# Optimization experiments

Hardware: AMD Instinct MI355X
Metric: run time of the kernel (lower is better)

Reference implementation:

```python
import jax, jax.numpy as jnp
import numpy as np

GAMMA = 0.5

def smooth_step(t, gamma=GAMMA):
    # DSelect-k SmoothStep: 0 below -g/2, 1 above g/2, cubic in between.
    tc = jnp.clip(t, -gamma / 2, gamma / 2)
    return (-2.0 / gamma**3) * tc**3 + (3.0 / (2.0 * gamma)) * tc + 0.5

def setup_inputs() -> dict:
    key = jax.random.key(0)
    k1, k2, k3 = jax.random.split(key, 3)
    B, p, k, m = 65536, 1024, 8, 6
    x = jax.random.normal(k1, (B, p), dtype=jnp.float32)
    G_w = jax.random.normal(k2, (k, p), dtype=jnp.float32) / np.sqrt(p)
    G_b = jnp.zeros((k,), dtype=jnp.float32)
    W_w = jax.random.normal(k3, (k * m, p), dtype=jnp.float32) / np.sqrt(p)
    W_b = jnp.zeros((k * m,), dtype=jnp.float32)
    return {"x": x, "G_w": G_w, "G_b": G_b, "W_w": W_w, "W_b": W_b}

def reference(x, G_w, G_b, W_w, W_b):
    B = x.shape[0]
    k = G_w.shape[0]
    m = W_w.shape[0] // k
    n = 2 ** m  # number of experts encoded by m binary gates
    gates = (x @ W_w.T + W_b).reshape(B, k, m)
    z = smooth_step(gates)  # (B, k, m) in [0, 1]
    # per_example_selector: probability of expert e = prod_j (z_j if bit_j(e) else 1-z_j)
    bits = ((np.arange(n)[:, None] >> np.arange(m)[None, :]) & 1).astype(bool)  # (n, m)
    bits = jnp.asarray(bits)
    sel = jnp.prod(jnp.where(bits[None, None, :, :], z[:, :, None, :], 1.0 - z[:, :, None, :]), axis=-1)  # (B, k, n)
    weights = jax.nn.softmax(x @ G_w.T + G_b, axis=1)  # (B, k)
    mixture = jnp.einsum('bk,bkn->bn', weights, sel)  # bmm((B,1,k),(B,k,n)) -> (B, n)
    return mixture
```

## Files before the change

kernel.cpp:

```cpp
#include <hip/hip_runtime.h>

typedef _Float16 half8 __attribute__((ext_vector_type(8)));
typedef float f32x4 __attribute__((ext_vector_type(4)));
typedef float f4 __attribute__((ext_vector_type(4)));

#define P_DIM 1024
#define BM 64
#define NH 8
#define AF_ROW 132

__global__ __launch_bounds__(256) void prep_weights(
    const float* __restrict__ Gw, const float* __restrict__ Gb,
    const float* __restrict__ Ww, const float* __restrict__ Wb,
    _Float16* __restrict__ Wf2, float* __restrict__ biasC) {
  int i = blockIdx.x * 256 + threadIdx.x;
  int j = i & 7;
  int l = (i >> 3) & 63;
  int t = (i >> 9) & 3;
  int S = i >> 11;
  int row = t * 16 + (l & 15);
  int k   = S * 32 + (l >> 4) * 8 + j;
  float v = 0.0f;
  if (row < 48) v = Ww[row * P_DIM + k];
  else if (row < 56) v = Gw[(row - 48) * P_DIM + k];
  Wf2[i] = (_Float16)v;
  if (i < 64) {
    float bv = 0.0f;
    if (i < 48) bv = Wb[i];
    else if (i < 56) bv = Gb[i - 48];
    biasC[i] = bv;
  }
}

#define BODY(cc) do { \
    half8 b0_ = *(const half8*)(BsR + (size_t)((2*(cc)  )*4    ) * 1024); \
    half8 b1_ = *(const half8*)(BsR + (size_t)((2*(cc)+1)*4    ) * 1024); \
    half8 b2_ = *(const half8*)(BsR + (size_t)((2*(cc)  )*4 + 1) * 1024); \
    half8 b3_ = *(const half8*)(BsR + (size_t)((2*(cc)+1)*4 + 1) * 1024); \
    f4 a0_[4], a1_[4]; \
    { const char* p0 = Abase0 + (cc) * 256; \
      a0_[0] = *(const f4*)(p0);       a0_[1] = *(const f4*)(p0 + 16); \
      a0_[2] = *(const f4*)(p0 + 128); a0_[3] = *(const f4*)(p0 + 144); \
      const char* p1 = Abase1 + (cc) * 256; \
      a1_[0] = *(const f4*)(p1);       a1_[1] = *(const f4*)(p1 + 16); \
      a1_[2] = *(const f4*)(p1 + 128); a1_[3] = *(const f4*)(p1 + 144); } \
    half8 h00_, h01_, h10_, h11_; \
    h00_[0]=(_Float16)a0_[0][0]; h00_[1]=(_Float16)a0_[0][1]; h00_[2]=(_Float16)a0_[0][2]; h00_[3]=(_Float16)a0_[0][3]; \
    h00_[4]=(_Float16)a0_[1][0]; h00_[5]=(_Float16)a0_[1][1]; h00_[6]=(_Float16)a0_[1][2]; h00_[7]=(_Float16)a0_[1][3]; \
    h01_[0]=(_Float16)a0_[2][0]; h01_[1]=(_Float16)a0_[2][1]; h01_[2]=(_Float16)a0_[2][2]; h01_[3]=(_Float16)a0_[2][3]; \
    h01_[4]=(_Float16)a0_[3][0]; h01_[5]=(_Float16)a0_[3][1]; h01_[6]=(_Float16)a0_[3][2]; h01_[7]=(_Float16)a0_[3][3]; \
    h10_[0]=(_Float16)a1_[0][0]; h10_[1]=(_Float16)a1_[0][1]; h10_[2]=(_Float16)a1_[0][2]; h10_[3]=(_Float16)a1_[0][3]; \
    h10_[4]=(_Float16)a1_[1][0]; h10_[5]=(_Float16)a1_[1][1]; h10_[6]=(_Float16)a1_[1][2]; h10_[7]=(_Float16)a1_[1][3]; \
    h11_[0]=(_Float16)a1_[2][0]; h11_[1]=(_Float16)a1_[2][1]; h11_[2]=(_Float16)a1_[2][2]; h11_[3]=(_Float16)a1_[2][3]; \
    h11_[4]=(_Float16)a1_[3][0]; h11_[5]=(_Float16)a1_[3][1]; h11_[6]=(_Float16)a1_[3][2]; h11_[7]=(_Float16)a1_[3][3]; \
    acc[0] = __builtin_amdgcn_mfma_f32_16x16x32_f16(h00_, b0_, acc[0], 0, 0, 0); \
    acc[0] = __builtin_amdgcn_mfma_f32_16x16x32_f16(h01_, b1_, acc[0], 0, 0, 0); \
    acc[1] = __builtin_amdgcn_mfma_f32_16x16x32_f16(h00_, b2_, acc[1], 0, 0, 0); \
    acc[1] = __builtin_amdgcn_mfma_f32_16x16x32_f16(h01_, b3_, acc[1], 0, 0, 0); \
    acc[2] = __builtin_amdgcn_mfma_f32_16x16x32_f16(h10_, b0_, acc[2], 0, 0, 0); \
    acc[2] = __builtin_amdgcn_mfma_f32_16x16x32_f16(h11_, b1_, acc[2], 0, 0, 0); \
    acc[3] = __builtin_amdgcn_mfma_f32_16x16x32_f16(h10_, b2_, acc[3], 0, 0, 0); \
    acc[3] = __builtin_amdgcn_mfma_f32_16x16x32_f16(h11_, b3_, acc[3], 0, 0, 0); \
  } while (0)

__global__ __launch_bounds__(256, 3) void fused_gate(
    const float* __restrict__ x, const _Float16* __restrict__ Wf2,
    const float* __restrict__ biasC, float* __restrict__ out) {
  __shared__ __align__(16) float Af[BM][AF_ROW];
  __shared__ __align__(16) _Float16 BsH[8192];

  const int tid  = threadIdx.x;
  const int lane = tid & 63;
  const int w    = tid >> 6;
  const int row0 = blockIdx.x * BM;
  const int l15  = lane & 15;
  const int q    = lane >> 4;

  const int mrow = (w >> 1) * 32;
  const int ncol = (w & 1) * 32;
  const int tb   = (w & 1) * 2;

  const char* xg = (const char*)(x + (size_t)(row0 + w * 16) * P_DIM) + lane * 8;
  const char* bgG = (const char*)Wf2 + (size_t)(w * 4) * 1024 + lane * 16;

  char* Aw = (char*)&Af[w * 16][0] + lane * 8;
  const char* Abase0 = (const char*)&Af[mrow + l15][0] + q * 32;
  const char* Abase1 = Abase0 + 16 * 528;
  char* BsW = (char*)BsH + (size_t)(w * 4) * 1024 + lane * 16;
  const char* BsR = (const char*)BsH + (size_t)tb * 1024 + lane * 16;

  f32x4 acc[4];
#pragma unroll
  for (int t = 0; t < 4; ++t) acc[t] = (f32x4){0.f, 0.f, 0.f, 0.f};

  float2 pf[16];
#pragma unroll
  for (int i = 0; i < 16; ++i) pf[i] = *(const float2*)(xg + i * 4096);
  half8 bR[4];
#pragma unroll
  for (int i = 0; i < 4; ++i) bR[i] = *(const half8*)(bgG + (size_t)i * 1024);

  for (int h = 0; h < NH; ++h) {
    if (h) __syncthreads();
#pragma unroll
    for (int i = 0; i < 16; ++i)
      *(float2*)(Aw + i * 528) = pf[i];
#pragma unroll
    for (int i = 0; i < 4; ++i)
      *(half8*)(BsW + (size_t)i * 1024) = bR[i];
    __syncthreads();
    if (h + 1 < NH) {
      const size_t boff = (size_t)(h + 1) * 16384;
#pragma unroll
      for (int i = 0; i < 4; ++i)
        bR[i] = *(const half8*)(bgG + boff + (size_t)i * 1024);
#pragma unroll
      for (int i = 0; i < 16; ++i)
        pf[i] = *(const float2*)(xg + i * 4096 + (h + 1) * 512);
    }
    BODY(0);
    BODY(1);
  }

  __syncthreads();
  float (*S)[65] = (float (*)[65])&Af[0][0];

#pragma unroll
  for (int m = 0; m < 2; ++m) {
#pragma unroll
    for (int j = 0; j < 2; ++j) {
      const int col = ncol + j * 16 + l15;
      float bias = biasC[col];
#pragma unroll
      for (int rr = 0; rr < 4; ++rr) {
        S[mrow + m * 16 + q * 4 + rr][col] = acc[m * 2 + j][rr] + bias;
      }
    }
  }
  __syncthreads();

  const int r2  = tid >> 2;
  const int sub = tid & 3;

  float lg[8];
#pragma unroll
  for (int k = 0; k < 8; ++k) lg[k] = S[r2][48 + k];
  float mx = lg[0];
#pragma unroll
  for (int k = 1; k < 8; ++k) mx = fmaxf(mx, lg[k]);
  float wk[8];
  float ssum = 0.f;
#pragma unroll
  for (int k = 0; k < 8; ++k) { wk[k] = expf(lg[k] - mx); ssum += wk[k]; }
  const float inv = 1.0f / ssum;

  float mix[16];
#pragma unroll
  for (int i = 0; i < 16; ++i) mix[i] = 0.f;

#pragma unroll
  for (int k = 0; k < 8; ++k) {
    float z[6];
#pragma unroll
    for (int j = 0; j < 6; ++j) {
      float tt = S[r2][k * 6 + j];
      float tc = fminf(fmaxf(tt, -0.25f), 0.25f);
      z[j] = fmaf(tc, fmaf(-16.0f * tc, tc, 3.0f), 0.5f);
    }
    float f4v = (sub & 1) ? z[4] : 1.0f - z[4];
    float f5v = (sub & 2) ? z[5] : 1.0f - z[5];
    float wf = wk[k] * inv * f4v * f5v;
    float t2[2], t4[4], t8[8], t16[16];
    t2[0] = 1.0f - z[0]; t2[1] = z[0];
#pragma unroll
    for (int i = 0; i < 2; ++i) { t4[i] = t2[i] * (1.0f - z[1]); t4[i + 2] = t2[i] * z[1]; }
#pragma unroll
    for (int i = 0; i < 4; ++i) { t8[i] = t4[i] * (1.0f - z[2]); t8[i + 4] = t4[i] * z[2]; }
#pragma unroll
    for (int i = 0; i < 8; ++i) { t16[i] = t8[i] * (1.0f - z[3]); t16[i + 8] = t8[i] * z[3]; }
#pragma unroll
    for (int i = 0; i < 16; ++i) mix[i] = fmaf(wf, t16[i], mix[i]);
  }

  float* op = out + (size_t)(row0 + r2) * 64 + sub * 16;
#pragma unroll
  for (int g = 0; g < 4; ++g) {
    float4 o;
    o.x = mix[4 * g + 0]; o.y = mix[4 * g + 1];
    o.z = mix[4 * g + 2]; o.w = mix[4 * g + 3];
    ((float4*)op)[g] = o;
  }
}

extern "C" void kernel_launch(void* const* d_in, const int* in_sizes, int n_in,
                              void* d_out, int out_size, void* d_ws, size_t ws_size,
                              hipStream_t stream) {
  const float* x  = (const float*)d_in[0];
  const float* Gw = (const float*)d_in[1];
  const float* Gb = (const float*)d_in[2];
  const float* Ww = (const float*)d_in[3];
  const float* Wb = (const float*)d_in[4];
  float* out = (float*)d_out;

  _Float16* Wf2  = (_Float16*)d_ws;
  float*    bias = (float*)((char*)d_ws + 64 * P_DIM * sizeof(_Float16));

  const int B = in_sizes[0] / P_DIM;

  prep_weights<<<dim3(256), dim3(256), 0, stream>>>(Gw, Gb, Ww, Wb, Wf2, bias);
  fused_gate<<<dim3(B / BM), dim3(256), 0, stream>>>(x, Wf2, bias, out);
  (void)n_in; (void)out_size; (void)ws_size;
}
```

Baseline: 57.58 us.

## Double-buffer x prefetch registers two stages ahead with manual barriers

Keeps two register sets of prefetched x chunks so global loads are issued two K-stages ahead instead of one, giving each load more time before its data is stored to LDS. The loop is fully unrolled into paired steps and uses explicit lgkmcnt waits with sched_barrier-fenced s_barrier instead of __syncthreads. This doubles the prefetch register footprint, which risks spills or lower occupancy under the launch bound of 3 blocks per CU.

```diff
diff --git a/kernel.cpp b/kernel.cpp
--- a/kernel.cpp
+++ b/kernel.cpp
@@ -63,6 +63,36 @@
     acc[3] = __builtin_amdgcn_mfma_f32_16x16x32_f16(h11_, b3_, acc[3], 0, 0, 0); \
   } while (0)
 
+#define SB() __builtin_amdgcn_sched_barrier(0)
+#define STEP(pf, h) do { \
+    asm volatile("s_waitcnt lgkmcnt(0)" ::: "memory"); \
+    SB(); \
+    __builtin_amdgcn_s_barrier(); \
+    SB(); \
+    _Pragma("unroll") \
+    for (int i_ = 0; i_ < 16; ++i_) \
+      *(float2*)(Aw + i_ * 528) = pf[i_]; \
+    _Pragma("unroll") \
+    for (int i_ = 0; i_ < 4; ++i_) \
+      *(half8*)(BsW + (size_t)i_ * 1024) = bR[i_]; \
+    asm volatile("s_waitcnt lgkmcnt(0)" ::: "memory"); \
+    SB(); \
+    __builtin_amdgcn_s_barrier(); \
+    SB(); \
+    if ((h) + 1 < NH) { \
+      _Pragma("unroll") \
+      for (int i_ = 0; i_ < 4; ++i_) \
+        bR[i_] = *(const half8*)(bgG + (size_t)((h) + 1) * 16384 + (size_t)i_ * 1024); \
+    } \
+    if ((h) + 2 < NH) { \
+      _Pragma("unroll") \
+      for (int i_ = 0; i_ < 16; ++i_) \
+        pf[i_] = *(const float2*)(xg + i_ * 4096 + ((h) + 2) * 512); \
+    } \
+    BODY(0); \
+    BODY(1); \
+  } while (0)
+
 __global__ __launch_bounds__(256, 3) void fused_gate(
     const float* __restrict__ x, const _Float16* __restrict__ Wf2,
     const float* __restrict__ biasC, float* __restrict__ out) {
@@ -93,33 +123,19 @@
 #pragma unroll
   for (int t = 0; t < 4; ++t) acc[t] = (f32x4){0.f, 0.f, 0.f, 0.f};
 
-  float2 pf[16];
-#pragma unroll
-  for (int i = 0; i < 16; ++i) pf[i] = *(const float2*)(xg + i * 4096);
   half8 bR[4];
 #pragma unroll
   for (int i = 0; i < 4; ++i) bR[i] = *(const half8*)(bgG + (size_t)i * 1024);
-
-  for (int h = 0; h < NH; ++h) {
-    if (h) __syncthreads();
-#pragma unroll
-    for (int i = 0; i < 16; ++i)
-      *(float2*)(Aw + i * 528) = pf[i];
-#pragma unroll
-    for (int i = 0; i < 4; ++i)
-      *(half8*)(BsW + (size_t)i * 1024) = bR[i];
-    __syncthreads();
-    if (h + 1 < NH) {
-      const size_t boff = (size_t)(h + 1) * 16384;
-#pragma unroll
-      for (int i = 0; i < 4; ++i)
-        bR[i] = *(const half8*)(bgG + boff + (size_t)i * 1024);
-#pragma unroll
-      for (int i = 0; i < 16; ++i)
-        pf[i] = *(const float2*)(xg + i * 4096 + (h + 1) * 512);
-    }
-    BODY(0);
-    BODY(1);
+  float2 pfA[16], pfB[16];
+#pragma unroll
+  for (int i = 0; i < 16; ++i) pfA[i] = *(const float2*)(xg + i * 4096);
+#pragma unroll
+  for (int i = 0; i < 16; ++i) pfB[i] = *(const float2*)(xg + i * 4096 + 512);
+
+#pragma unroll
+  for (int hh = 0; hh < NH; hh += 2) {
+    STEP(pfA, hh);
+    STEP(pfB, hh + 1);
   }
 
   __syncthreads();
```

New measurement: 65.02 us. +12.9%, slower.
